# Kernel optimization log

Hardware: AMD Instinct MI355X
Metric: run time of the kernel (lower is better)

Reference implementation:

```python
import jax, jax.numpy as jnp
import numpy as np

N = 262144            # number of particles
H0 = 0.006            # base SPH support radius (unit square domain)
GRID = 256            # static upper bound on cells per dimension (actual ~170)
NUM_CELLS = GRID * GRID
K = 32                # max particles stored per cell (avg occupancy ~9.4)
NCAND = 9 * K         # searchRadius=1 -> 3x3 cell stencil
MAX_NEIGHBORS = 64    # padded neighbor-list width (avg neighbor count ~27)


def setup_inputs() -> dict:
    key = jax.random.key(0)
    kp, ks = jax.random.split(key)
    positions = jax.random.uniform(kp, (N, 2), dtype=jnp.float32)
    # supports in [0.9*H0, H0], mimicking mildly adaptive SPH supports
    supports = H0 * (0.9 + 0.1 * jax.random.uniform(ks, (N,), dtype=jnp.float32))
    return {"positions": positions, "supports": supports}


def _cell_linear_indices(positions, supports):
    # mirrors sortPositions: cell size = hMax, indices = ceil((p - qMin)/hMax)
    hMax = jnp.max(supports)
    qMin = jnp.min(positions, axis=0) - hMax
    ij = jnp.ceil((positions - qMin) / hMax).astype(jnp.int32)  # >= 1 by construction
    ij = jnp.clip(ij, 0, GRID - 1)
    return ij[:, 0] + GRID * ij[:, 1]


def _build_cell_table(lin):
    # dense equivalent of the hash-grid: sort by cell, counting-sort into [cell, slot]
    order = jnp.argsort(lin)                       # == sortingIndices in the original
    lin_s = lin[order]
    counts = jax.ops.segment_sum(jnp.ones(N, jnp.int32), lin, num_segments=NUM_CELLS)
    starts = jnp.cumsum(counts) - counts           # exclusive prefix sum == cumCell
    rank = jnp.arange(N, dtype=jnp.int32) - starts[lin_s].astype(jnp.int32)
    ovf = rank >= K                                # overflow slots -> dump row
    cell_t = jnp.where(ovf, NUM_CELLS, lin_s)
    slot_t = jnp.where(ovf, 0, rank)
    table = jnp.full((NUM_CELLS + 1, K), -1, dtype=jnp.int32)
    table = table.at[cell_t, slot_t].set(order.astype(jnp.int32))
    return table


def reference(positions, supports):
    lin = _cell_linear_indices(positions, supports)
    table = _build_cell_table(lin)

    # 3x3 stencil of neighbor cells (searchRadius = 1)
    dx, dy = jnp.meshgrid(jnp.arange(-1, 2), jnp.arange(-1, 2), indexing='ij')
    offs = (dx + GRID * dy).reshape(1, 9).astype(jnp.int32)
    cand_cells = jnp.clip(lin[:, None] + offs, 0, NUM_CELLS)  # [N, 9]

    cand = table[cand_cells].reshape(N, NCAND)     # [N, 288] candidate particle ids
    present = cand >= 0
    cidx = jnp.where(present, cand, 0)
    cpos = positions[cidx]                         # [N, 288, 2] gather (memory bound)
    diff = cpos - positions[:, None, :]
    dist = jnp.sqrt(jnp.sum(diff * diff, axis=-1)) # [N, 288]
    valid = present & (dist <= supports[:, None])  # |x_i - x_j| <= h_i (self included)
    count = jnp.sum(valid, axis=1).astype(jnp.int32)

    # compact valid candidates to the front, pad to MAX_NEIGHBORS
    order2 = jnp.argsort(jnp.where(valid, 0, 1).astype(jnp.int32), axis=1, stable=True)
    sel = order2[:, :MAX_NEIGHBORS]
    nbr = jnp.take_along_axis(cidx, sel, axis=1)
    dsel = jnp.take_along_axis(dist, sel, axis=1)
    inb = jnp.arange(MAX_NEIGHBORS)[None, :] < count[:, None]
    neighbors = jnp.where(inb, nbr, -1)
    radial = jnp.where(inb, dsel / supports[:, None], 0.0)  # fluidRadialDistances
    return neighbors, count, radial
```

## Files before the change

### kernel.cpp

```cpp
#include <hip/hip_runtime.h>
#include <float.h>

#define N_PART 262144
#define GRID_DIM 256
#define NUM_CELLS (GRID_DIM * GRID_DIM)
#define KSLOT 32
#define MAXNB 64


__global__ void init_params(unsigned int* params) {
    params[0] = 0x7f7fffffu;
    params[1] = 0x7f7fffffu;
    params[2] = 0u;
}

__global__ void reduce_kernel(const float* __restrict__ pos,
                              const float* __restrict__ sup,
                              unsigned int* params, int n) {
    __shared__ unsigned int s_minx, s_miny, s_maxh;
    if (threadIdx.x == 0) { s_minx = 0x7f7fffffu; s_miny = 0x7f7fffffu; s_maxh = 0u; }
    __syncthreads();
    const float2* pos2 = (const float2*)pos;
    float mx = FLT_MAX, my = FLT_MAX, mh = 0.0f;
    for (int i = blockIdx.x * blockDim.x + threadIdx.x; i < n;
         i += gridDim.x * blockDim.x) {
        float2 p = pos2[i];
        float h = sup[i];
        mx = fminf(mx, p.x);
        my = fminf(my, p.y);
        mh = fmaxf(mh, h);
    }
    atomicMin(&s_minx, __float_as_uint(mx));
    atomicMin(&s_miny, __float_as_uint(my));
    atomicMax(&s_maxh, __float_as_uint(mh));
    __syncthreads();
    if (threadIdx.x == 0) {
        atomicMin(&params[0], s_minx);
        atomicMin(&params[1], s_miny);
        atomicMax(&params[2], s_maxh);
    }
}

__global__ void bin_kernel(const float* __restrict__ pos,
                           const unsigned int* __restrict__ params,
                           int* __restrict__ counts, int* __restrict__ lin_out,
                           int n) {
    int i = blockIdx.x * blockDim.x + threadIdx.x;
    if (i >= n) return;
    float hmax  = __uint_as_float(params[2]);
    float qminx = __uint_as_float(params[0]) - hmax;
    float qminy = __uint_as_float(params[1]) - hmax;
    float2 p = ((const float2*)pos)[i];
    int cx = (int)ceilf((p.x - qminx) / hmax);
    int cy = (int)ceilf((p.y - qminy) / hmax);
    cx = min(max(cx, 0), GRID_DIM - 1);
    cy = min(max(cy, 0), GRID_DIM - 1);
    int lin = cx + GRID_DIM * cy;
    lin_out[i] = lin;
    atomicAdd(&counts[lin], 1);
}

__global__ void scan_local(const int* __restrict__ counts,
                           int* __restrict__ starts,
                           int* __restrict__ chunkSums) {
    __shared__ int sd[256];
    int t = threadIdx.x;
    int idx = blockIdx.x * 256 + t;
    int v = counts[idx];
    sd[t] = v;
    __syncthreads();
#pragma unroll
    for (int off = 1; off < 256; off <<= 1) {
        int x = (t >= off) ? sd[t - off] : 0;
        __syncthreads();
        sd[t] += x;
        __syncthreads();
    }
    starts[idx] = sd[t] - v;
    if (t == 255) chunkSums[blockIdx.x] = sd[t];
}

__global__ void scan_apply(int* __restrict__ starts,
                           const int* __restrict__ chunkSums, int n) {
    __shared__ int red[256];
    int t = threadIdx.x, b = blockIdx.x;
    red[t] = (t < b) ? chunkSums[t] : 0;
    __syncthreads();
#pragma unroll
    for (int s = 128; s > 0; s >>= 1) {
        if (t < s) red[t] += red[t + s];
        __syncthreads();
    }
    starts[b * 256 + t] += red[0];
    if (b == 255 && t == 0) {
        starts[NUM_CELLS]     = n;
        starts[NUM_CELLS + 1] = n;
    }
}

__global__ void scatter_kernel(const int* __restrict__ lin,
                               const int* __restrict__ starts,
                               int* __restrict__ cursor,
                               int* __restrict__ sid, int n) {
    int i = blockIdx.x * blockDim.x + threadIdx.x;
    if (i >= n) return;
    int c = lin[i];
    int r = atomicAdd(&cursor[c], 1);
    sid[starts[c] + r] = i;
}

__global__ void sortseg_kernel(const int* __restrict__ starts,
                               const int* __restrict__ sid,
                               int* __restrict__ linS,
                               float4* __restrict__ Q,
                               const float2* __restrict__ pos2,
                               const float* __restrict__ sup) {
    int c = blockIdx.x * blockDim.x + threadIdx.x;
    if (c >= NUM_CELLS) return;
    int b = starts[c], e = starts[c + 1];
    int prev = -1;
    for (int k = b; k < e; k++) {
        int best = 0x7fffffff;
        for (int s = b; s < e; s++) {
            int v = sid[s];
            best = (v > prev && v < best) ? v : best;
        }
        prev = best;
        float2 pj = pos2[best];
        Q[k] = make_float4(pj.x, pj.y, __int_as_float(best), sup[best]);
        linS[k] = c;
    }
}

__global__ __launch_bounds__(256) void query_kernel(
        const int* __restrict__ linS, const float4* __restrict__ Q,
        const int* __restrict__ starts,
        float* __restrict__ outN, float* __restrict__ outC,
        float* __restrict__ outR, int n) {
#pragma clang fp contract(off)
    __shared__ int   s_id[4][MAXNB];
    __shared__ float s_s2[4][MAXNB];

    int gtid = blockIdx.x * blockDim.x + threadIdx.x;
    int r    = gtid >> 6;
    int lane = threadIdx.x & 63;
    int wsl  = threadIdx.x >> 6;

    float4 me = Q[r];
    int   i  = __builtin_amdgcn_readfirstlane(__float_as_int(me.z));
    float px = __int_as_float(__builtin_amdgcn_readfirstlane(__float_as_int(me.x)));
    float py = __int_as_float(__builtin_amdgcn_readfirstlane(__float_as_int(me.y)));
    float h  = __int_as_float(__builtin_amdgcn_readfirstlane(__float_as_int(me.w)));
    int   L  = __builtin_amdgcn_readfirstlane(linS[r]);

    float  hn  = __int_as_float(__float_as_int(h) + 1);
    double mid = 0.5 * ((double)h + (double)hn);
    double t2  = mid * mid;
    float  S   = (float)t2;
    S = ((double)S > t2) ? __int_as_float(__float_as_int(S) - 1) : S;

    const int offs[9] = {-257, -1, 255, -256, 0, 256, -255, 1, 257};
    int cum[10], delta[9];
    cum[0] = 0;
#pragma unroll
    for (int o = 0; o < 9; o++) {
        int cell = L + offs[o];
        cell = min(max(cell, 0), NUM_CELLS);
        int bb = __builtin_amdgcn_readfirstlane(starts[cell]);
        int ee = __builtin_amdgcn_readfirstlane(starts[cell + 1]);
        int cc = min(ee - bb, KSLOT);
        delta[o]  = bb - cum[o];
        cum[o + 1] = cum[o] + cc;
    }
    int T = cum[9];

    int total = 0;
    for (int b0 = 0; b0 < T; b0 += 64) {
        int ll = b0 + lane;
        int dsel = delta[0];
#pragma unroll
        for (int m = 1; m < 9; m++)
            dsel = (ll >= cum[m]) ? delta[m] : dsel;
        int idx = ll + dsel;
        float4 q = Q[idx];
        float dx = q.x - px;
        float dy = q.y - py;
        float s2 = dx * dx + dy * dy;
        int rem = T - b0;
        unsigned long long maskT =
            (rem >= 64) ? ~0ull : ((1ull << rem) - 1ull);
        unsigned long long bal = __ballot(s2 <= S) & maskT;
        int rank = __builtin_amdgcn_mbcnt_hi(
            (unsigned)(bal >> 32),
            __builtin_amdgcn_mbcnt_lo((unsigned)bal, 0));
        int w = total + rank;
        if ((s2 <= S) && (ll < T) && (w < MAXNB)) {
            s_id[wsl][w] = __float_as_int(q.z);
            s_s2[wsl][w] = s2;
        }
        total += (int)__popcll(bal);
    }

    int stored = min(total, MAXNB);
    float rh = __builtin_amdgcn_rcpf(h);
    size_t base = (size_t)i * MAXNB;
    int   jj = s_id[wsl][lane];
    float ss = s_s2[wsl][lane];
    bool inb = lane < stored;
    float vN = inb ? (float)jj : -1.0f;
    float vR = inb ? __builtin_amdgcn_sqrtf(ss) * rh : 0.0f;
    outN[base + lane] = vN;
    outR[base + lane] = vR;
    if (lane == 0) outC[i] = (float)total;
}

extern "C" void kernel_launch(void* const* d_in, const int* in_sizes, int n_in,
                              void* d_out, int out_size, void* d_ws, size_t ws_size,
                              hipStream_t stream) {
    const float* pos = (const float*)d_in[0];
    const float* sup = (const float*)d_in[1];

    char* p = (char*)d_ws;
    auto alloc = [&](size_t bytes) {
        char* q = p;
        p += (bytes + 255) & ~(size_t)255;
        return q;
    };
    unsigned int* params    = (unsigned int*)alloc(256);
    int*          counts    = (int*)alloc((size_t)NUM_CELLS * 4);
    int*          cursor    = (int*)alloc((size_t)NUM_CELLS * 4);
    int*          chunkSums = (int*)alloc(256 * 4);
    int*          starts    = (int*)alloc((size_t)(NUM_CELLS + 2) * 4);
    int*          lin       = (int*)alloc((size_t)N_PART * 4);
    int*          sid       = (int*)alloc((size_t)(N_PART + 64) * 4);
    int*          linS      = (int*)alloc((size_t)N_PART * 4);
    float4*       Q         = (float4*)alloc((size_t)(N_PART + 64) * 16);

    float* out  = (float*)d_out;
    float* outN = out;
    float* outC = out + (size_t)N_PART * MAXNB;
    float* outR = outC + N_PART;

    hipMemsetAsync(counts, 0, (size_t)NUM_CELLS * 4 * 2, stream);
    init_params<<<1, 1, 0, stream>>>(params);
    reduce_kernel<<<256, 256, 0, stream>>>(pos, sup, params, N_PART);
    bin_kernel<<<N_PART / 256, 256, 0, stream>>>(pos, params, counts, lin, N_PART);
    scan_local<<<NUM_CELLS / 256, 256, 0, stream>>>(counts, starts, chunkSums);
    scan_apply<<<NUM_CELLS / 256, 256, 0, stream>>>(starts, chunkSums, N_PART);
    scatter_kernel<<<N_PART / 256, 256, 0, stream>>>(lin, starts, cursor, sid, N_PART);
    sortseg_kernel<<<NUM_CELLS / 256, 256, 0, stream>>>(starts, sid, linS, Q,
                                                        (const float2*)pos, sup);
    query_kernel<<<(N_PART * 64) / 256, 256, 0, stream>>>(
        linS, Q, starts, outN, outC, outR, N_PART);
}
```

Measured before the change: 309.1 us.

## Fuse grid-build pipeline into one cooperative kernel and swizzle query blocks

Merges the memset, reduction, binning, two-level scan, scatter and per-cell sort into a single cooperative kernel that uses grid-wide syncs instead of separate launches. This removes several kernel launch gaps and the memset. The per-cell sort becomes a rank-by-count placement instead of repeated min-selection. The query kernel also remaps block indices with a swizzle to change the traversal order. Grid syncs on 256 blocks add barrier cost, and the per-cell sort work stays serial per thread.

```diff
diff --git a/kernel.cpp b/kernel.cpp
--- a/kernel.cpp
+++ b/kernel.cpp
@@ -1,134 +1,139 @@
 #include <hip/hip_runtime.h>
+#include <hip/hip_cooperative_groups.h>
 #include <float.h>
+
+namespace cg = cooperative_groups;
 
 #define N_PART 262144
 #define GRID_DIM 256
 #define NUM_CELLS (GRID_DIM * GRID_DIM)
 #define KSLOT 32
 #define MAXNB 64
-
-
-__global__ void init_params(unsigned int* params) {
-    params[0] = 0x7f7fffffu;
-    params[1] = 0x7f7fffffu;
-    params[2] = 0u;
-}
-
-__global__ void reduce_kernel(const float* __restrict__ pos,
-                              const float* __restrict__ sup,
-                              unsigned int* params, int n) {
-    __shared__ unsigned int s_minx, s_miny, s_maxh;
-    if (threadIdx.x == 0) { s_minx = 0x7f7fffffu; s_miny = 0x7f7fffffu; s_maxh = 0u; }
-    __syncthreads();
-    const float2* pos2 = (const float2*)pos;
-    float mx = FLT_MAX, my = FLT_MAX, mh = 0.0f;
-    for (int i = blockIdx.x * blockDim.x + threadIdx.x; i < n;
-         i += gridDim.x * blockDim.x) {
+#define BLD_BLOCKS 256
+#define BLD_TPB 256
+#define BLD_NT (BLD_BLOCKS * BLD_TPB)
+
+
+__global__ __launch_bounds__(BLD_TPB) void build_kernel(
+        const float2* __restrict__ pos2, const float* __restrict__ sup,
+        int* counts, int* cursor, int* chunkSums, int* chunkOff,
+        int* starts, int* lin, int* sid, int* linS, float4* Q,
+        float* blockMinX, float* blockMinY, float* blockMaxH) {
+    cg::grid_group grid = cg::this_grid();
+    __shared__ unsigned s_minx, s_miny, s_maxh;
+    __shared__ int sd[256];
+
+    int t   = threadIdx.x;
+    int b   = blockIdx.x;
+    int tid = b * BLD_TPB + t;
+
+    counts[tid] = 0;
+    cursor[tid] = 0;
+    if (t == 0) { s_minx = 0x7f7fffffu; s_miny = 0x7f7fffffu; s_maxh = 0u; }
+    __syncthreads();
+    {
+        float mx = FLT_MAX, my = FLT_MAX, mh = 0.0f;
+#pragma unroll
+        for (int k = 0; k < N_PART / BLD_NT; k++) {
+            int i = tid + k * BLD_NT;
+            float2 p = pos2[i];
+            float h = sup[i];
+            mx = fminf(mx, p.x);
+            my = fminf(my, p.y);
+            mh = fmaxf(mh, h);
+        }
+        atomicMin(&s_minx, __float_as_uint(mx));
+        atomicMin(&s_miny, __float_as_uint(my));
+        atomicMax(&s_maxh, __float_as_uint(mh));
+    }
+    __syncthreads();
+    if (t == 0) {
+        blockMinX[b] = __uint_as_float(s_minx);
+        blockMinY[b] = __uint_as_float(s_miny);
+        blockMaxH[b] = __uint_as_float(s_maxh);
+    }
+    grid.sync();
+
+    if (t == 0) { s_minx = 0x7f7fffffu; s_miny = 0x7f7fffffu; s_maxh = 0u; }
+    __syncthreads();
+    atomicMin(&s_minx, __float_as_uint(blockMinX[t]));
+    atomicMin(&s_miny, __float_as_uint(blockMinY[t]));
+    atomicMax(&s_maxh, __float_as_uint(blockMaxH[t]));
+    __syncthreads();
+    float hmax  = __uint_as_float(s_maxh);
+    float qminx = __uint_as_float(s_minx) - hmax;
+    float qminy = __uint_as_float(s_miny) - hmax;
+#pragma unroll
+    for (int k = 0; k < N_PART / BLD_NT; k++) {
+        int i = tid + k * BLD_NT;
         float2 p = pos2[i];
-        float h = sup[i];
-        mx = fminf(mx, p.x);
-        my = fminf(my, p.y);
-        mh = fmaxf(mh, h);
-    }
-    atomicMin(&s_minx, __float_as_uint(mx));
-    atomicMin(&s_miny, __float_as_uint(my));
-    atomicMax(&s_maxh, __float_as_uint(mh));
-    __syncthreads();
-    if (threadIdx.x == 0) {
-        atomicMin(&params[0], s_minx);
-        atomicMin(&params[1], s_miny);
-        atomicMax(&params[2], s_maxh);
-    }
-}
-
-__global__ void bin_kernel(const float* __restrict__ pos,
-                           const unsigned int* __restrict__ params,
-                           int* __restrict__ counts, int* __restrict__ lin_out,
-                           int n) {
-    int i = blockIdx.x * blockDim.x + threadIdx.x;
-    if (i >= n) return;
-    float hmax  = __uint_as_float(params[2]);
-    float qminx = __uint_as_float(params[0]) - hmax;
-    float qminy = __uint_as_float(params[1]) - hmax;
-    float2 p = ((const float2*)pos)[i];
-    int cx = (int)ceilf((p.x - qminx) / hmax);
-    int cy = (int)ceilf((p.y - qminy) / hmax);
-    cx = min(max(cx, 0), GRID_DIM - 1);
-    cy = min(max(cy, 0), GRID_DIM - 1);
-    int lin = cx + GRID_DIM * cy;
-    lin_out[i] = lin;
-    atomicAdd(&counts[lin], 1);
-}
-
-__global__ void scan_local(const int* __restrict__ counts,
-                           int* __restrict__ starts,
-                           int* __restrict__ chunkSums) {
-    __shared__ int sd[256];
-    int t = threadIdx.x;
-    int idx = blockIdx.x * 256 + t;
-    int v = counts[idx];
-    sd[t] = v;
-    __syncthreads();
-#pragma unroll
-    for (int off = 1; off < 256; off <<= 1) {
-        int x = (t >= off) ? sd[t - off] : 0;
+        int cx = (int)ceilf((p.x - qminx) / hmax);
+        int cy = (int)ceilf((p.y - qminy) / hmax);
+        cx = min(max(cx, 0), GRID_DIM - 1);
+        cy = min(max(cy, 0), GRID_DIM - 1);
+        int l = cx + GRID_DIM * cy;
+        lin[i] = l;
+        atomicAdd(&counts[l], 1);
+    }
+    grid.sync();
+
+    {
+        int v = counts[tid];
+        sd[t] = v;
         __syncthreads();
-        sd[t] += x;
+#pragma unroll
+        for (int off = 1; off < 256; off <<= 1) {
+            int x = (t >= off) ? sd[t - off] : 0;
+            __syncthreads();
+            sd[t] += x;
+            __syncthreads();
+        }
+        starts[tid] = sd[t] - v;
+        if (t == 255) chunkSums[b] = sd[t];
+    }
+    grid.sync();
+
+    if (b == 0) {
+        int cv = chunkSums[t];
+        sd[t] = cv;
         __syncthreads();
-    }
-    starts[idx] = sd[t] - v;
-    if (t == 255) chunkSums[blockIdx.x] = sd[t];
-}
-
-__global__ void scan_apply(int* __restrict__ starts,
-                           const int* __restrict__ chunkSums, int n) {
-    __shared__ int red[256];
-    int t = threadIdx.x, b = blockIdx.x;
-    red[t] = (t < b) ? chunkSums[t] : 0;
-    __syncthreads();
-#pragma unroll
-    for (int s = 128; s > 0; s >>= 1) {
-        if (t < s) red[t] += red[t + s];
-        __syncthreads();
-    }
-    starts[b * 256 + t] += red[0];
-    if (b == 255 && t == 0) {
-        starts[NUM_CELLS]     = n;
-        starts[NUM_CELLS + 1] = n;
-    }
-}
-
-__global__ void scatter_kernel(const int* __restrict__ lin,
-                               const int* __restrict__ starts,
-                               int* __restrict__ cursor,
-                               int* __restrict__ sid, int n) {
-    int i = blockIdx.x * blockDim.x + threadIdx.x;
-    if (i >= n) return;
-    int c = lin[i];
-    int r = atomicAdd(&cursor[c], 1);
-    sid[starts[c] + r] = i;
-}
-
-__global__ void sortseg_kernel(const int* __restrict__ starts,
-                               const int* __restrict__ sid,
-                               int* __restrict__ linS,
-                               float4* __restrict__ Q,
-                               const float2* __restrict__ pos2,
-                               const float* __restrict__ sup) {
-    int c = blockIdx.x * blockDim.x + threadIdx.x;
-    if (c >= NUM_CELLS) return;
-    int b = starts[c], e = starts[c + 1];
-    int prev = -1;
-    for (int k = b; k < e; k++) {
-        int best = 0x7fffffff;
-        for (int s = b; s < e; s++) {
-            int v = sid[s];
-            best = (v > prev && v < best) ? v : best;
-        }
-        prev = best;
-        float2 pj = pos2[best];
-        Q[k] = make_float4(pj.x, pj.y, __int_as_float(best), sup[best]);
-        linS[k] = c;
+#pragma unroll
+        for (int off = 1; off < 256; off <<= 1) {
+            int x = (t >= off) ? sd[t - off] : 0;
+            __syncthreads();
+            sd[t] += x;
+            __syncthreads();
+        }
+        chunkOff[t] = sd[t] - cv;
+    }
+    grid.sync();
+
+    starts[tid] += chunkOff[b];
+    if (tid == 0) {
+        starts[NUM_CELLS]     = N_PART;
+        starts[NUM_CELLS + 1] = N_PART;
+    }
+    grid.sync();
+
+#pragma unroll
+    for (int k = 0; k < N_PART / BLD_NT; k++) {
+        int i = tid + k * BLD_NT;
+        int c = lin[i];
+        int r = atomicAdd(&cursor[c], 1);
+        sid[starts[c] + r] = i;
+    }
+    grid.sync();
+
+    {
+        int bb = starts[tid], ee = starts[tid + 1];
+        for (int k = bb; k < ee; k++) {
+            int val = sid[k];
+            int rank = 0;
+            for (int s = bb; s < ee; s++) rank += (sid[s] < val);
+            float2 pj = pos2[val];
+            Q[bb + rank] = make_float4(pj.x, pj.y, __int_as_float(val), sup[val]);
+            linS[bb + rank] = tid;
+        }
     }
 }
 
@@ -141,7 +146,9 @@
     __shared__ int   s_id[4][MAXNB];
     __shared__ float s_s2[4][MAXNB];
 
-    int gtid = blockIdx.x * blockDim.x + threadIdx.x;
+    int bid = blockIdx.x;
+    int swz = (bid & 7) * (int)(gridDim.x >> 3) + (bid >> 3);
+    int gtid = swz * 256 + threadIdx.x;
     int r    = gtid >> 6;
     int lane = threadIdx.x & 63;
     int wsl  = threadIdx.x >> 6;
@@ -217,8 +224,8 @@
 extern "C" void kernel_launch(void* const* d_in, const int* in_sizes, int n_in,
                               void* d_out, int out_size, void* d_ws, size_t ws_size,
                               hipStream_t stream) {
-    const float* pos = (const float*)d_in[0];
-    const float* sup = (const float*)d_in[1];
+    const float2* pos2 = (const float2*)d_in[0];
+    const float*  sup  = (const float*)d_in[1];
 
     char* p = (char*)d_ws;
     auto alloc = [&](size_t bytes) {
@@ -226,30 +233,30 @@
         p += (bytes + 255) & ~(size_t)255;
         return q;
     };
-    unsigned int* params    = (unsigned int*)alloc(256);
-    int*          counts    = (int*)alloc((size_t)NUM_CELLS * 4);
-    int*          cursor    = (int*)alloc((size_t)NUM_CELLS * 4);
-    int*          chunkSums = (int*)alloc(256 * 4);
-    int*          starts    = (int*)alloc((size_t)(NUM_CELLS + 2) * 4);
-    int*          lin       = (int*)alloc((size_t)N_PART * 4);
-    int*          sid       = (int*)alloc((size_t)(N_PART + 64) * 4);
-    int*          linS      = (int*)alloc((size_t)N_PART * 4);
-    float4*       Q         = (float4*)alloc((size_t)(N_PART + 64) * 16);
+    int*    counts    = (int*)alloc((size_t)NUM_CELLS * 4);
+    int*    cursor    = (int*)alloc((size_t)NUM_CELLS * 4);
+    int*    chunkSums = (int*)alloc(256 * 4);
+    int*    chunkOff  = (int*)alloc(256 * 4);
+    int*    starts    = (int*)alloc((size_t)(NUM_CELLS + 2) * 4);
+    int*    lin       = (int*)alloc((size_t)N_PART * 4);
+    int*    sid       = (int*)alloc((size_t)(N_PART + 64) * 4);
+    int*    linS      = (int*)alloc((size_t)N_PART * 4);
+    float4* Q         = (float4*)alloc((size_t)(N_PART + 64) * 16);
+    float*  blockMinX = (float*)alloc(256 * 4);
+    float*  blockMinY = (float*)alloc(256 * 4);
+    float*  blockMaxH = (float*)alloc(256 * 4);
 
     float* out  = (float*)d_out;
     float* outN = out;
     float* outC = out + (size_t)N_PART * MAXNB;
     float* outR = outC + N_PART;
 
-    hipMemsetAsync(counts, 0, (size_t)NUM_CELLS * 4 * 2, stream);
-    init_params<<<1, 1, 0, stream>>>(params);
-    reduce_kernel<<<256, 256, 0, stream>>>(pos, sup, params, N_PART);
-    bin_kernel<<<N_PART / 256, 256, 0, stream>>>(pos, params, counts, lin, N_PART);
-    scan_local<<<NUM_CELLS / 256, 256, 0, stream>>>(counts, starts, chunkSums);
-    scan_apply<<<NUM_CELLS / 256, 256, 0, stream>>>(starts, chunkSums, N_PART);
-    scatter_kernel<<<N_PART / 256, 256, 0, stream>>>(lin, starts, cursor, sid, N_PART);
-    sortseg_kernel<<<NUM_CELLS / 256, 256, 0, stream>>>(starts, sid, linS, Q,
-                                                        (const float2*)pos, sup);
+    void* args[] = { (void*)&pos2, (void*)&sup, (void*)&counts, (void*)&cursor,
+                     (void*)&chunkSums, (void*)&chunkOff, (void*)&starts,
+                     (void*)&lin, (void*)&sid, (void*)&linS, (void*)&Q,
+                     (void*)&blockMinX, (void*)&blockMinY, (void*)&blockMaxH };
+    hipLaunchCooperativeKernel((const void*)build_kernel, dim3(BLD_BLOCKS),
+                               dim3(BLD_TPB), args, 0, stream);
     query_kernel<<<(N_PART * 64) / 256, 256, 0, stream>>>(
         linS, Q, starts, outN, outC, outR, N_PART);
 }
```

Result: slower. 449.9 us (+45.5%).
